# Optimization experiments

Hardware: AMD Instinct MI355X
Metric: run time of the kernel (lower is better)

## Reference

```python
import jax, jax.numpy as jnp
import numpy as np

M = 8      # quantization steps
K = 256    # codewords per step
D = 128    # vector dim
H = 256    # hidden dim of residual MLP
S = M - 1  # number of neural steps (steps 1..M-1)
L = 2      # residual blocks per step
BEAM = 16  # beam width (cfg.B)
A = 8      # substep shortlist size (n_codes)
B = 2048   # batch


def setup_inputs() -> dict:
    key = jax.random.key(0)
    ks = jax.random.split(key, 16)
    sc = 0.05
    f32 = jnp.float32
    return {
        "x": jax.random.normal(ks[0], (B, D), f32),
        "codebook": jax.random.normal(ks[1], (M, K, D), f32) * sc,
        "codebook_rq": jax.random.normal(ks[2], (S, K, D), f32) * sc,
        "W_in": jax.random.normal(ks[3], (S, D, H), f32) * (D ** -0.5),
        "b_in": jnp.zeros((S, H), f32),
        "W_cat": jax.random.normal(ks[4], (S, H + D, H), f32) * ((H + D) ** -0.5),
        "b_cat": jnp.zeros((S, H), f32),
        "W1": jax.random.normal(ks[5], (S, L, H, H), f32) * (H ** -0.5),
        "b1": jnp.zeros((S, L, H), f32),
        "W2": jax.random.normal(ks[6], (S, L, H, H), f32) * (H ** -0.5),
        "b2": jnp.zeros((S, L, H), f32),
        "W_out": jax.random.normal(ks[7], (S, H, D), f32) * (H ** -0.5),
        "b_out": jnp.zeros((S, D), f32),
    }


def _approx_dist(q, cb):
    # approx squared L2 dist, dropping the query norm: ||c||^2 - 2 q.c
    # q: (..., D), cb: (K, D) -> (..., K)
    return jnp.sum(cb * cb, axis=-1) - 2.0 * q @ cb.T


def reference(x, codebook, codebook_rq, W_in, b_in, W_cat, b_cat,
              W1, b1, W2, b2, W_out, b_out):
    # --- step 0: plain codebook lookup, keep top-BEAM candidates ---
    d0 = _approx_dist(x, codebook[0])                  # (B, K)
    _, codes0 = jax.lax.top_k(-d0, BEAM)               # (B, BEAM) smallest dists
    xhat = codebook[0][codes0]                          # (B, BEAM, D)
    codes_list = [codes0]

    for s in range(S):
        i_step = s + 1
        F_in = xhat.shape[1]
        F_out = BEAM if i_step < M - 1 else 1

        # substep pre-filter: shortlist A codes per beam element
        xt = x[:, None, :] - xhat                      # (B, F, D)
        d = _approx_dist(xt, codebook_rq[s])           # (B, F, K)
        _, top_c = jax.lax.top_k(-d, A)                # (B, F, A)
        cw = codebook[i_step][top_c]                   # gather: (B, F, A, D)
        cw_res = cw

        # residual MLP conditioned on current xhat
        h = cw @ W_in[s] + b_in[s]                     # (B, F, A, H)
        xb = jnp.broadcast_to(xhat[:, :, None, :], cw.shape)
        h = jnp.concatenate([h, xb], axis=-1) @ W_cat[s] + b_cat[s]
        for l in range(L):
            h = h + jax.nn.relu(h @ W1[s, l] + b1[s, l]) @ W2[s, l] + b2[s, l]
        cw = h @ W_out[s] + b_out[s] + cw_res          # res_codeword_coeff = 1.0

        # re-score flattened beam*shortlist candidates and prune to F_out
        cand = (cw + xhat[:, :, None, :]).reshape(B, F_in * A, D)
        d2 = jnp.sum(cand * cand, axis=-1) - 2.0 * jnp.einsum('bd,bkd->bk', x, cand)
        _, idx = jax.lax.top_k(-d2, F_out)             # (B, F_out)

        parent = idx // A                               # == repeat_interleave+gather
        codes_list = [jnp.take_along_axis(c, parent, axis=-1) for c in codes_list]
        codes_list.append(jnp.take_along_axis(top_c.reshape(B, F_in * A), idx, axis=-1))
        xhat = jnp.take_along_axis(cand, idx[:, :, None], axis=1)  # (B, F_out, D)

    codes_MB = jnp.stack([c[:, 0] for c in codes_list])  # (M, B), final beam = 1
    return codes_MB, xhat[:, 0, :]
```

## Files before the change

### kernel.cpp

```cpp
#include <hip/hip_runtime.h>
#include <float.h>

#define BB    2048
#define DD    128
#define KK    256
#define HH    256
#define MM    8
#define SS    7
#define BEAMW 16
#define AA    8
#define WM    32

typedef _Float16 f16x8 __attribute__((ext_vector_type(8)));
typedef float    f32x4 __attribute__((ext_vector_type(4)));

#define HSWZ(row, m) (((row) << 5) + ((((m) + ((((row) >> 3)) << 2))) & 31))

__device__ __forceinline__ int hoff(int m, int j) {
  return m * 256 + ((((j >> 3) ^ (m & 7)) << 3) | (j & 7));
}

__global__ __launch_bounds__(64) void step0_kernel(
    const float* __restrict__ x, const float* __restrict__ cb,
    float* __restrict__ xhat, int* __restrict__ codes)
{
  int b = blockIdx.x, l = threadIdx.x;
  __shared__ float xs[DD];
  xs[l]      = x[b * DD + l];
  xs[l + 64] = x[b * DD + 64 + l];
  __syncthreads();
  float dist[4];
#pragma unroll
  for (int q = 0; q < 4; ++q) {
    const float* row = cb + (size_t)(q * 64 + l) * DD;
    float dot = 0.f, nrm = 0.f;
#pragma unroll 8
    for (int d = 0; d < DD; d += 4) {
      float4 c = *(const float4*)(row + d);
      dot += c.x * xs[d] + c.y * xs[d + 1] + c.z * xs[d + 2] + c.w * xs[d + 3];
      nrm += c.x * c.x + c.y * c.y + c.z * c.z + c.w * c.w;
    }
    dist[q] = nrm - 2.f * dot;
  }
  for (int it = 0; it < BEAMW; ++it) {
    float bv = dist[0]; int bi = l;
#pragma unroll
    for (int q = 1; q < 4; ++q) {
      if (dist[q] < bv) { bv = dist[q]; bi = q * 64 + l; }
    }
#pragma unroll
    for (int mmk = 1; mmk < 64; mmk <<= 1) {
      float ov = __shfl_xor(bv, mmk);
      int   oi = __shfl_xor(bi, mmk);
      if (ov < bv || (ov == bv && oi < bi)) { bv = ov; bi = oi; }
    }
    const float* crow = cb + (size_t)bi * DD;
    float2 v = *(const float2*)(crow + l * 2);
    *(float2*)(xhat + (size_t)(b * BEAMW + it) * DD + l * 2) = v;
    if (l == 0) codes[(b * BEAMW + it) * MM] = bi;
    if (l == (bi & 63)) dist[bi >> 6] = FLT_MAX;
  }
}

__global__ __launch_bounds__(128) void rqprep_kernel(
    const float* __restrict__ rq, float* __restrict__ rqT, float* __restrict__ rqn)
{
  int k = blockIdx.x, d = threadIdx.x;
  float v = rq[k * DD + d];
  rqT[d * KK + k] = v;
  float p = v * v;
#pragma unroll
  for (int mmk = 1; mmk < 64; mmk <<= 1) p += __shfl_xor(p, mmk);
  __shared__ float ps[2];
  if ((d & 63) == 0) ps[d >> 6] = p;
  __syncthreads();
  if (d == 0) rqn[k] = ps[0] + ps[1];
}

__global__ __launch_bounds__(256) void codeterm_kernel(
    const float* __restrict__ cbstep, const float* __restrict__ Win,
    const float* __restrict__ bin, const float* __restrict__ Wcat,
    const float* __restrict__ bcat, float* __restrict__ ct)
{
  int k = blockIdx.x, j = threadIdx.x;
  __shared__ float crow[DD];
  __shared__ float h1[HH];
  if (j < DD) crow[j] = cbstep[k * DD + j];
  __syncthreads();
  float a = bin[j];
  for (int d = 0; d < DD; ++d) a += crow[d] * Win[d * HH + j];
  h1[j] = a;
  __syncthreads();
  float c = bcat[j];
  for (int t = 0; t < HH; ++t) c += h1[t] * Wcat[t * HH + j];
  ct[k * HH + j] = c;
}

__global__ __launch_bounds__(256) void wpack_kernel(
    const float* __restrict__ W1s, const float* __restrict__ W2s,
    const float* __restrict__ Wouts, const float* __restrict__ Wcat2s,
    _Float16* __restrict__ wAh, _Float16* __restrict__ wAl,
    _Float16* __restrict__ woh, _Float16* __restrict__ wol,
    _Float16* __restrict__ wch, _Float16* __restrict__ wcl)
{
  int t = blockIdx.x * 256 + threadIdx.x;
  const float* src; _Float16 *dh, *dl;
  int N, r;
  if (t < 32768) {
    int mi = t >> 13; r = t & 8191;
    src = (mi & 1 ? W2s : W1s) + (size_t)(mi >> 1) * HH * HH;
    dh = wAh + (size_t)mi * 65536; dl = wAl + (size_t)mi * 65536;
    N = 256;
  } else if (t < 36864) {
    r = t - 32768; src = Wouts; dh = woh; dl = wol; N = 128;
  } else {
    r = t - 36864; src = Wcat2s; dh = wch; dl = wcl; N = 256;
  }
  int l = r & 63;
  int nct = N >> 4;
  int c = (r >> 6) & (nct - 1);
  int q = r / (64 * nct);
  int k0 = q * 32 + (l >> 4) * 8;
  int col = c * 16 + (l & 15);
  size_t fo = (size_t)r * 8;
#pragma unroll
  for (int j = 0; j < 8; ++j) {
    float v = src[(size_t)(k0 + j) * N + col];
    _Float16 hi = (_Float16)v;
    dh[fo + j] = hi;
    dl[fo + j] = (_Float16)((v - (float)hi) * 2048.0f);
  }
}

__global__ __launch_bounds__(256) void prefilter_kernel(
    const float* __restrict__ x, const float* __restrict__ xhat,
    const float* __restrict__ rqT, const float* __restrict__ rqn,
    int* __restrict__ topc)
{
  __shared__ float xtT[DD * 32];
  __shared__ float distb[32 * KK];
  int tid = threadIdx.x;
  int bf0 = blockIdx.x * 32;
  for (int i = 0; i < 16; ++i) {
    int idx = tid + i * 256;
    int d = idx >> 5, r = idx & 31;
    int bf = bf0 + r;
    xtT[HSWZ(d, r)] = x[(bf >> 4) * DD + d] - xhat[(size_t)bf * DD + d];
  }
  __syncthreads();
  int jb = tid & 31, mb = tid >> 5;
  float acc[4][8];
#pragma unroll
  for (int i = 0; i < 4; ++i)
#pragma unroll
    for (int jj = 0; jj < 8; ++jj) acc[i][jj] = 0.f;
  for (int d = 0; d < DD; ++d) {
    float4 hv = *(float4*)&xtT[HSWZ(d, mb * 4)];
    float4 w0 = *(const float4*)&rqT[d * KK + jb * 8];
    float4 w1 = *(const float4*)&rqT[d * KK + jb * 8 + 4];
    float hvv[4] = {hv.x, hv.y, hv.z, hv.w};
    float wv[8]  = {w0.x, w0.y, w0.z, w0.w, w1.x, w1.y, w1.z, w1.w};
#pragma unroll
    for (int i = 0; i < 4; ++i)
#pragma unroll
      for (int jj = 0; jj < 8; ++jj) acc[i][jj] += hvv[i] * wv[jj];
  }
#pragma unroll
  for (int i = 0; i < 4; ++i) {
    int r = mb * 4 + i;
#pragma unroll
    for (int jj = 0; jj < 8; ++jj) {
      int k = jb * 8 + jj;
      distb[r * KK + k] = rqn[k] - 2.f * acc[i][jj];
    }
  }
  __syncthreads();
  int wv2 = tid >> 6, lane = tid & 63;
  for (int rr = 0; rr < 8; ++rr) {
    int r = wv2 * 8 + rr;
    float v[4];
#pragma unroll
    for (int q = 0; q < 4; ++q) v[q] = distb[r * KK + lane + q * 64];
    int bfr = bf0 + r;
    for (int it = 0; it < AA; ++it) {
      float bv = v[0]; int bi = lane;
#pragma unroll
      for (int q = 1; q < 4; ++q) {
        if (v[q] < bv) { bv = v[q]; bi = q * 64 + lane; }
      }
#pragma unroll
      for (int mmk = 1; mmk < 64; mmk <<= 1) {
        float ov = __shfl_xor(bv, mmk);
        int   oi = __shfl_xor(bi, mmk);
        if (ov < bv || (ov == bv && oi < bi)) { bv = ov; bi = oi; }
      }
      if (lane == (bi & 63)) v[bi >> 6] = FLT_MAX;
      if (lane == 0) topc[bfr * AA + it] = bi;
    }
  }
}

__global__ __launch_bounds__(512, 4) void mlp_kernel(
    const float* __restrict__ x, const float* __restrict__ xhat,
    const int* __restrict__ topc, const float* __restrict__ ct,
    const float* __restrict__ cbstep,
    const _Float16* __restrict__ wAh, const _Float16* __restrict__ wAl,
    const _Float16* __restrict__ woh, const _Float16* __restrict__ wol,
    const _Float16* __restrict__ wch, const _Float16* __restrict__ wcl,
    const float* __restrict__ b1a, const float* __restrict__ b2a,
    const float* __restrict__ bout,
    float* __restrict__ cand, float* __restrict__ d2g)
{
  __shared__ _Float16 hhi[WM * 256], hlo[WM * 256];
  __shared__ _Float16 xhh[16 * 128], xhl[16 * 128];
  __shared__ float xt[4 * 256];
  __shared__ float xs[DD];
  __shared__ float pd2[WM][8];
  __shared__ int   cl[WM];

  int tid = threadIdx.x;
  int l = tid & 63, w = tid >> 6;
  int lg = l >> 4, lr = l & 15;
  int bf0 = blockIdx.x * 4;
  int b = bf0 >> 4;
  const f32x4 z4 = {0.f, 0.f, 0.f, 0.f};

  if (tid < WM) cl[tid] = topc[bf0 * AA + tid];
  if (tid < DD) xs[tid] = x[b * DD + tid];
  for (int e = tid; e < 2048; e += 512) {
    int row = e >> 7, d = e & 127;
    float v = (row < 4) ? xhat[(size_t)(bf0 + row) * DD + d] : 0.f;
    _Float16 hi = (_Float16)v;
    xhh[e] = hi;
    xhl[e] = (_Float16)((v - (float)hi) * 2048.0f);
  }
  __syncthreads();

  {
    f32x4 ax1[2], ax2[2];
    ax1[0] = z4; ax1[1] = z4; ax2[0] = z4; ax2[1] = z4;
    for (int q = 0; q < 4; ++q) {
      int aoff = lr * 128 + q * 32 + lg * 8;
      f16x8 Ah = *(f16x8*)&xhh[aoff];
      f16x8 Al = *(f16x8*)&xhl[aoff];
#pragma unroll
      for (int c2 = 0; c2 < 2; ++c2) {
        size_t boff = ((size_t)(q * 16 + w * 2 + c2) * 64 + l) * 8;
        f16x8 Bh = *(const f16x8*)&wch[boff];
        f16x8 Bl = *(const f16x8*)&wcl[boff];
        ax1[c2] = __builtin_amdgcn_mfma_f32_16x16x32_f16(Ah, Bh, ax1[c2], 0, 0, 0);
        ax2[c2] = __builtin_amdgcn_mfma_f32_16x16x32_f16(Al, Bh, ax2[c2], 0, 0, 0);
        ax2[c2] = __builtin_amdgcn_mfma_f32_16x16x32_f16(Ah, Bl, ax2[c2], 0, 0, 0);
      }
    }
    if (l < 16) {
#pragma unroll
      for (int c2 = 0; c2 < 2; ++c2) {
        int j = (w * 2 + c2) * 16 + lr;
#pragma unroll
        for (int r = 0; r < 4; ++r)
          xt[r * 256 + j] = ax1[c2][r] + ax2[c2][r] * (1.0f / 2048.0f);
      }
    }
  }
  __syncthreads();

  for (int i = 0; i < 16; ++i) {
    int e = tid + i * 512;
    int m = e >> 8, j = e & 255;
    float v = ct[cl[m] * HH + j] + xt[(m >> 3) * 256 + j];
    _Float16 hi = (_Float16)v;
    int off = hoff(m, j);
    hhi[off] = hi;
    hlo[off] = (_Float16)((v - (float)hi) * 2048.0f);
  }
  __syncthreads();

  int j0 = (w * 2) * 16 + lr;
  int j1 = (w * 2 + 1) * 16 + lr;

  for (int lay = 0; lay < 2; ++lay) {
    const _Float16* W1h = wAh + (size_t)(lay * 2 + 0) * 65536;
    const _Float16* W1l = wAl + (size_t)(lay * 2 + 0) * 65536;
    const _Float16* W2h = wAh + (size_t)(lay * 2 + 1) * 65536;
    const _Float16* W2l = wAl + (size_t)(lay * 2 + 1) * 65536;
    const float* bb1 = b1a + lay * HH;
    const float* bb2 = b2a + lay * HH;

    f32x4 a1[2][2], a2[2][2];
#pragma unroll
    for (int rt = 0; rt < 2; ++rt)
#pragma unroll
      for (int c = 0; c < 2; ++c) { a1[rt][c] = z4; a2[rt][c] = z4; }
    for (int q = 0; q < 8; ++q) {
      f16x8 Bh[2], Bl[2];
#pragma unroll
      for (int c = 0; c < 2; ++c) {
        size_t boff = ((size_t)(q * 16 + w * 2 + c) * 64 + l) * 8;
        Bh[c] = *(const f16x8*)&W1h[boff];
        Bl[c] = *(const f16x8*)&W1l[boff];
      }
#pragma unroll
      for (int rt = 0; rt < 2; ++rt) {
        int arow = rt * 16 + lr;
        int aoff = arow * 256 + (((q * 4 + lg) ^ (arow & 7)) << 3);
        f16x8 Ah = *(f16x8*)&hhi[aoff];
        f16x8 Al = *(f16x8*)&hlo[aoff];
#pragma unroll
        for (int c = 0; c < 2; ++c) {
          a1[rt][c] = __builtin_amdgcn_mfma_f32_16x16x32_f16(Ah, Bh[c], a1[rt][c], 0, 0, 0);
          a2[rt][c] = __builtin_amdgcn_mfma_f32_16x16x32_f16(Al, Bh[c], a2[rt][c], 0, 0, 0);
          a2[rt][c] = __builtin_amdgcn_mfma_f32_16x16x32_f16(Ah, Bl[c], a2[rt][c], 0, 0, 0);
        }
      }
    }
#pragma unroll
    for (int rt = 0; rt < 2; ++rt)
#pragma unroll
      for (int c = 0; c < 2; ++c) {
        int j = (c == 0) ? j0 : j1;
        float bj = bb1[j];
#pragma unroll
        for (int r = 0; r < 4; ++r) {
          int m = rt * 16 + lg * 4 + r;
          float u = fmaxf(a1[rt][c][r] + a2[rt][c][r] * (1.0f / 2048.0f) + bj, 0.f);
          int off = hoff(m, j);
          float res = (float)hhi[off] + (float)hlo[off] * (1.0f / 2048.0f);
          a1[rt][c][r] = u;
          a2[rt][c][r] = res;
        }
      }
    __syncthreads();
#pragma unroll
    for (int rt = 0; rt < 2; ++rt)
#pragma unroll
      for (int c = 0; c < 2; ++c) {
        int j = (c == 0) ? j0 : j1;
#pragma unroll
        for (int r = 0; r < 4; ++r) {
          int m = rt * 16 + lg * 4 + r;
          float v = a1[rt][c][r];
          _Float16 hi = (_Float16)v;
          int off = hoff(m, j);
          hhi[off] = hi;
          hlo[off] = (_Float16)((v - (float)hi) * 2048.0f);
        }
      }
    __syncthreads();

#pragma unroll
    for (int rt = 0; rt < 2; ++rt)
#pragma unroll
      for (int c = 0; c < 2; ++c) {
        a1[rt][c] = a2[rt][c];
        a2[rt][c] = z4;
      }
    for (int q = 0; q < 8; ++q) {
      f16x8 Bh[2], Bl[2];
#pragma unroll
      for (int c = 0; c < 2; ++c) {
        size_t boff = ((size_t)(q * 16 + w * 2 + c) * 64 + l) * 8;
        Bh[c] = *(const f16x8*)&W2h[boff];
        Bl[c] = *(const f16x8*)&W2l[boff];
      }
#pragma unroll
      for (int rt = 0; rt < 2; ++rt) {
        int arow = rt * 16 + lr;
        int aoff = arow * 256 + (((q * 4 + lg) ^ (arow & 7)) << 3);
        f16x8 Ah = *(f16x8*)&hhi[aoff];
        f16x8 Al = *(f16x8*)&hlo[aoff];
#pragma unroll
        for (int c = 0; c < 2; ++c) {
          a1[rt][c] = __builtin_amdgcn_mfma_f32_16x16x32_f16(Ah, Bh[c], a1[rt][c], 0, 0, 0);
          a2[rt][c] = __builtin_amdgcn_mfma_f32_16x16x32_f16(Al, Bh[c], a2[rt][c], 0, 0, 0);
          a2[rt][c] = __builtin_amdgcn_mfma_f32_16x16x32_f16(Ah, Bl[c], a2[rt][c], 0, 0, 0);
        }
      }
    }
#pragma unroll
    for (int rt = 0; rt < 2; ++rt)
#pragma unroll
      for (int c = 0; c < 2; ++c) {
        int j = (c == 0) ? j0 : j1;
        float bj = bb2[j];
#pragma unroll
        for (int r = 0; r < 4; ++r)
          a1[rt][c][r] += a2[rt][c][r] * (1.0f / 2048.0f) + bj;
      }
    __syncthreads();
#pragma unroll
    for (int rt = 0; rt < 2; ++rt)
#pragma unroll
      for (int c = 0; c < 2; ++c) {
        int j = (c == 0) ? j0 : j1;
#pragma unroll
        for (int r = 0; r < 4; ++r) {
          int m = rt * 16 + lg * 4 + r;
          float v = a1[rt][c][r];
          _Float16 hi = (_Float16)v;
          int off = hoff(m, j);
          hhi[off] = hi;
          hlo[off] = (_Float16)((v - (float)hi) * 2048.0f);
        }
      }
    __syncthreads();
  }

  f32x4 o1[2], o2[2];
  o1[0] = z4; o1[1] = z4; o2[0] = z4; o2[1] = z4;
  for (int q = 0; q < 8; ++q) {
    size_t boff = ((size_t)(q * 8 + w) * 64 + l) * 8;
    f16x8 Bh = *(const f16x8*)&woh[boff];
    f16x8 Bl = *(const f16x8*)&wol[boff];
#pragma unroll
    for (int rt = 0; rt < 2; ++rt) {
      int arow = rt * 16 + lr;
      int aoff = arow * 256 + (((q * 4 + lg) ^ (arow & 7)) << 3);
      f16x8 Ah = *(f16x8*)&hhi[aoff];
      f16x8 Al = *(f16x8*)&hlo[aoff];
      o1[rt] = __builtin_amdgcn_mfma_f32_16x16x32_f16(Ah, Bh, o1[rt], 0, 0, 0);
      o2[rt] = __builtin_amdgcn_mfma_f32_16x16x32_f16(Al, Bh, o2[rt], 0, 0, 0);
      o2[rt] = __builtin_amdgcn_mfma_f32_16x16x32_f16(Ah, Bl, o2[rt], 0, 0, 0);
    }
  }
  int ci0 = (blockIdx.x & 3) * WM;
  int d = w * 16 + lr;
  float bo = bout[d];
  float xsd = xs[d];
#pragma unroll
  for (int rt = 0; rt < 2; ++rt) {
    float p[4];
#pragma unroll
    for (int r = 0; r < 4; ++r) {
      int m = rt * 16 + lg * 4 + r;
      float v = o1[rt][r] + o2[rt][r] * (1.0f / 2048.0f) + bo
              + cbstep[(size_t)cl[m] * DD + d]
              + xhat[(size_t)(bf0 + (m >> 3)) * DD + d];
      cand[((size_t)(b * 128 + ci0 + m)) * DD + d] = v;
      p[r] = v * (v - 2.f * xsd);
    }
#pragma unroll
    for (int mk = 1; mk < 16; mk <<= 1) {
#pragma unroll
      for (int r = 0; r < 4; ++r) p[r] += __shfl_xor(p[r], mk);
    }
    if (lr == 0) {
#pragma unroll
      for (int r = 0; r < 4; ++r) pd2[rt * 16 + lg * 4 + r][w] = p[r];
    }
  }
  __syncthreads();
  if (tid < WM) {
    float s = 0.f;
#pragma unroll
    for (int ww = 0; ww < 8; ++ww) s += pd2[tid][ww];
    d2g[b * 128 + ci0 + tid] = s;
  }
}

__global__ __launch_bounds__(64) void topk_update_kernel(
    const float* __restrict__ d2g, const float* __restrict__ cand,
    const int* __restrict__ codes_in, const int* __restrict__ topc,
    float* __restrict__ xhat_out, int* __restrict__ codes_out,
    int fout, int spos)
{
  int b = blockIdx.x, lane = threadIdx.x;
  float v0 = d2g[b * 128 + lane];
  float v1 = d2g[b * 128 + 64 + lane];
  for (int r = 0; r < fout; ++r) {
    float bv = v0; int bi = lane;
    if (v1 < bv) { bv = v1; bi = 64 + lane; }
#pragma unroll
    for (int mmk = 1; mmk < 64; mmk <<= 1) {
      float ov = __shfl_xor(bv, mmk);
      int   oi = __shfl_xor(bi, mmk);
      if (ov < bv || (ov == bv && oi < bi)) { bv = ov; bi = oi; }
    }
    int parent = bi >> 3, a = bi & 7;
    if (lane < MM) {
      int valc = (lane == spos) ? topc[(b * BEAMW + parent) * AA + a]
                                : codes_in[(b * BEAMW + parent) * MM + lane];
      codes_out[(b * BEAMW + r) * MM + lane] = valc;
    }
    const float* src = cand + ((size_t)(b * 128 + bi)) * DD;
    float2 t = *(const float2*)(src + lane * 2);
    *(float2*)(xhat_out + (size_t)(b * BEAMW + r) * DD + lane * 2) = t;
    if (bi < 64) { if (lane == bi) v0 = FLT_MAX; }
    else         { if (lane == bi - 64) v1 = FLT_MAX; }
  }
}

__global__ __launch_bounds__(64) void finalize_kernel(
    const int* __restrict__ codes_fin, const float* __restrict__ xhat_fin,
    float* __restrict__ out)
{
  int b = blockIdx.x, lane = threadIdx.x;
  float2 t = *(const float2*)(xhat_fin + (size_t)(b * BEAMW) * DD + lane * 2);
  *(float2*)(out + (size_t)MM * BB + (size_t)b * DD + lane * 2) = t;
  if (lane < MM) out[lane * BB + b] = (float)codes_fin[(b * BEAMW) * MM + lane];
}

extern "C" void kernel_launch(void* const* d_in, const int* in_sizes, int n_in,
                              void* d_out, int out_size, void* d_ws, size_t ws_size,
                              hipStream_t stream)
{
  (void)in_sizes; (void)n_in; (void)out_size; (void)ws_size;
  const float* x    = (const float*)d_in[0];
  const float* cb   = (const float*)d_in[1];
  const float* rq   = (const float*)d_in[2];
  const float* Win  = (const float*)d_in[3];
  const float* bin  = (const float*)d_in[4];
  const float* Wcat = (const float*)d_in[5];
  const float* bcat = (const float*)d_in[6];
  const float* W1   = (const float*)d_in[7];
  const float* b1   = (const float*)d_in[8];
  const float* W2   = (const float*)d_in[9];
  const float* b2   = (const float*)d_in[10];
  const float* Wout = (const float*)d_in[11];
  const float* bout = (const float*)d_in[12];
  float* out = (float*)d_out;

  char* ws = (char*)d_ws;
  size_t off = 0;
  auto alloc = [&](size_t bytes) -> void* {
    void* p = ws + off;
    off += (bytes + 255) & ~(size_t)255;
    return p;
  };
  float* X0    = (float*)alloc((size_t)BB * BEAMW * DD * 4);
  float* X1    = (float*)alloc((size_t)BB * BEAMW * DD * 4);
  int*   C0    = (int*)  alloc((size_t)BB * BEAMW * MM * 4);
  int*   C1    = (int*)  alloc((size_t)BB * BEAMW * MM * 4);
  int*   tc    = (int*)  alloc((size_t)BB * BEAMW * AA * 4);
  float* rqT   = (float*)alloc((size_t)DD * KK * 4);
  float* rqn   = (float*)alloc((size_t)KK * 4);
  float* ct    = (float*)alloc((size_t)KK * HH * 4);
  float* d2b   = (float*)alloc((size_t)BB * 128 * 4);
  float* candb = (float*)alloc((size_t)BB * 128 * DD * 4);
  _Float16* wAh = (_Float16*)alloc((size_t)4 * 65536 * 2);
  _Float16* wAl = (_Float16*)alloc((size_t)4 * 65536 * 2);
  _Float16* woh = (_Float16*)alloc((size_t)32768 * 2);
  _Float16* wol = (_Float16*)alloc((size_t)32768 * 2);
  _Float16* wch = (_Float16*)alloc((size_t)32768 * 2);
  _Float16* wcl = (_Float16*)alloc((size_t)32768 * 2);

  step0_kernel<<<BB, 64, 0, stream>>>(x, cb, X0, C0);
  float* Xc = X0; float* Xn = X1;
  int* Cc = C0; int* Cn = C1;
  for (int s = 0; s < SS; ++s) {
    wpack_kernel<<<160, 256, 0, stream>>>(
        W1 + (size_t)s * 2 * HH * HH, W2 + (size_t)s * 2 * HH * HH,
        Wout + (size_t)s * HH * DD,
        Wcat + (size_t)s * 384 * HH + (size_t)256 * HH,
        wAh, wAl, woh, wol, wch, wcl);
    rqprep_kernel<<<KK, DD, 0, stream>>>(rq + (size_t)s * KK * DD, rqT, rqn);
    codeterm_kernel<<<KK, HH, 0, stream>>>(cb + (size_t)(s + 1) * KK * DD,
        Win + (size_t)s * DD * HH, bin + (size_t)s * HH,
        Wcat + (size_t)s * 384 * HH, bcat + (size_t)s * HH, ct);
    prefilter_kernel<<<(BB * BEAMW) / 32, 256, 0, stream>>>(x, Xc, rqT, rqn, tc);
    mlp_kernel<<<(BB * BEAMW * AA) / WM, 512, 0, stream>>>(x, Xc, tc, ct,
        cb + (size_t)(s + 1) * KK * DD,
        wAh, wAl, woh, wol, wch, wcl,
        b1 + (size_t)s * 2 * HH, b2 + (size_t)s * 2 * HH,
        bout + (size_t)s * DD,
        candb, d2b);
    int fo = (s < SS - 1) ? BEAMW : 1;
    topk_update_kernel<<<BB, 64, 0, stream>>>(d2b, candb, Cc, tc, Xn, Cn, fo, s + 1);
    { float* t = Xc; Xc = Xn; Xn = t; }
    { int* t = Cc; Cc = Cn; Cn = t; }
  }
  finalize_kernel<<<BB, 64, 0, stream>>>(Cc, Xc, out);
}
```

Baseline: 4.870 ms.

## Hoist xhat W_cat term into separate kernel and double MLP rows per block

Moves the xhat·W_cat projection out of the MLP kernel into a new xterm kernel that computes it once per beam row with full 16-row MFMA tiles, instead of padding 4 rows to 16 inside each MLP block. The MLP kernel now processes 64 candidate rows per block instead of 32, so each weight fragment loaded from global memory feeds twice as many MFMAs. The cost is an extra launch, a global round trip for the xterm buffer, twice the LDS for the hidden state, and more accumulator registers, which may lower occupancy.

```diff
diff --git a/kernel.cpp b/kernel.cpp
--- a/kernel.cpp
+++ b/kernel.cpp
@@ -9,7 +9,7 @@
 #define SS    7
 #define BEAMW 16
 #define AA    8
-#define WM    32
+#define WM    64
 
 typedef _Float16 f16x8 __attribute__((ext_vector_type(8)));
 typedef float    f32x4 __attribute__((ext_vector_type(4)));
@@ -132,6 +132,52 @@
   }
 }
 
+__global__ __launch_bounds__(256) void xterm_kernel(
+    const float* __restrict__ xhat,
+    const _Float16* __restrict__ wch, const _Float16* __restrict__ wcl,
+    float* __restrict__ xtg)
+{
+  int tid = threadIdx.x;
+  int l = tid & 63, w = tid >> 6;
+  int lg = l >> 4, lr = l & 15;
+  int r0 = blockIdx.x * 16;
+  const f32x4 z4 = {0.f, 0.f, 0.f, 0.f};
+  f32x4 a1[4], a2[4];
+#pragma unroll
+  for (int c = 0; c < 4; ++c) { a1[c] = z4; a2[c] = z4; }
+  for (int q = 0; q < 4; ++q) {
+    const float* ap = xhat + (size_t)(r0 + lr) * DD + q * 32 + lg * 8;
+    float4 f0 = *(const float4*)ap;
+    float4 f1 = *(const float4*)(ap + 4);
+    float fv[8] = {f0.x, f0.y, f0.z, f0.w, f1.x, f1.y, f1.z, f1.w};
+    f16x8 Ah, Al;
+#pragma unroll
+    for (int j = 0; j < 8; ++j) {
+      _Float16 hi = (_Float16)fv[j];
+      Ah[j] = hi;
+      Al[j] = (_Float16)((fv[j] - (float)hi) * 2048.0f);
+    }
+#pragma unroll
+    for (int c = 0; c < 4; ++c) {
+      size_t boff = ((size_t)(q * 16 + w * 4 + c) * 64 + l) * 8;
+      f16x8 Bh = *(const f16x8*)&wch[boff];
+      f16x8 Bl = *(const f16x8*)&wcl[boff];
+      a1[c] = __builtin_amdgcn_mfma_f32_16x16x32_f16(Ah, Bh, a1[c], 0, 0, 0);
+      a2[c] = __builtin_amdgcn_mfma_f32_16x16x32_f16(Al, Bh, a2[c], 0, 0, 0);
+      a2[c] = __builtin_amdgcn_mfma_f32_16x16x32_f16(Ah, Bl, a2[c], 0, 0, 0);
+    }
+  }
+#pragma unroll
+  for (int c = 0; c < 4; ++c) {
+    int col = (w * 4 + c) * 16 + lr;
+#pragma unroll
+    for (int r = 0; r < 4; ++r) {
+      int row = r0 + lg * 4 + r;
+      xtg[(size_t)row * 256 + col] = a1[c][r] + a2[c][r] * (1.0f / 2048.0f);
+    }
+  }
+}
+
 __global__ __launch_bounds__(256) void prefilter_kernel(
     const float* __restrict__ x, const float* __restrict__ xhat,
     const float* __restrict__ rqT, const float* __restrict__ rqn,
@@ -203,17 +249,14 @@
 __global__ __launch_bounds__(512, 4) void mlp_kernel(
     const float* __restrict__ x, const float* __restrict__ xhat,
     const int* __restrict__ topc, const float* __restrict__ ct,
-    const float* __restrict__ cbstep,
+    const float* __restrict__ cbstep, const float* __restrict__ xtg,
     const _Float16* __restrict__ wAh, const _Float16* __restrict__ wAl,
     const _Float16* __restrict__ woh, const _Float16* __restrict__ wol,
-    const _Float16* __restrict__ wch, const _Float16* __restrict__ wcl,
     const float* __restrict__ b1a, const float* __restrict__ b2a,
     const float* __restrict__ bout,
     float* __restrict__ cand, float* __restrict__ d2g)
 {
   __shared__ _Float16 hhi[WM * 256], hlo[WM * 256];
-  __shared__ _Float16 xhh[16 * 128], xhl[16 * 128];
-  __shared__ float xt[4 * 256];
   __shared__ float xs[DD];
   __shared__ float pd2[WM][8];
   __shared__ int   cl[WM];
@@ -221,54 +264,18 @@
   int tid = threadIdx.x;
   int l = tid & 63, w = tid >> 6;
   int lg = l >> 4, lr = l & 15;
-  int bf0 = blockIdx.x * 4;
+  int bf0 = blockIdx.x * 8;
   int b = bf0 >> 4;
   const f32x4 z4 = {0.f, 0.f, 0.f, 0.f};
 
   if (tid < WM) cl[tid] = topc[bf0 * AA + tid];
   if (tid < DD) xs[tid] = x[b * DD + tid];
-  for (int e = tid; e < 2048; e += 512) {
-    int row = e >> 7, d = e & 127;
-    float v = (row < 4) ? xhat[(size_t)(bf0 + row) * DD + d] : 0.f;
-    _Float16 hi = (_Float16)v;
-    xhh[e] = hi;
-    xhl[e] = (_Float16)((v - (float)hi) * 2048.0f);
-  }
-  __syncthreads();
-
-  {
-    f32x4 ax1[2], ax2[2];
-    ax1[0] = z4; ax1[1] = z4; ax2[0] = z4; ax2[1] = z4;
-    for (int q = 0; q < 4; ++q) {
-      int aoff = lr * 128 + q * 32 + lg * 8;
-      f16x8 Ah = *(f16x8*)&xhh[aoff];
-      f16x8 Al = *(f16x8*)&xhl[aoff];
-#pragma unroll
-      for (int c2 = 0; c2 < 2; ++c2) {
-        size_t boff = ((size_t)(q * 16 + w * 2 + c2) * 64 + l) * 8;
-        f16x8 Bh = *(const f16x8*)&wch[boff];
-        f16x8 Bl = *(const f16x8*)&wcl[boff];
-        ax1[c2] = __builtin_amdgcn_mfma_f32_16x16x32_f16(Ah, Bh, ax1[c2], 0, 0, 0);
-        ax2[c2] = __builtin_amdgcn_mfma_f32_16x16x32_f16(Al, Bh, ax2[c2], 0, 0, 0);
-        ax2[c2] = __builtin_amdgcn_mfma_f32_16x16x32_f16(Ah, Bl, ax2[c2], 0, 0, 0);
-      }
-    }
-    if (l < 16) {
-#pragma unroll
-      for (int c2 = 0; c2 < 2; ++c2) {
-        int j = (w * 2 + c2) * 16 + lr;
-#pragma unroll
-        for (int r = 0; r < 4; ++r)
-          xt[r * 256 + j] = ax1[c2][r] + ax2[c2][r] * (1.0f / 2048.0f);
-      }
-    }
-  }
-  __syncthreads();
-
-  for (int i = 0; i < 16; ++i) {
+  __syncthreads();
+
+  for (int i = 0; i < 32; ++i) {
     int e = tid + i * 512;
     int m = e >> 8, j = e & 255;
-    float v = ct[cl[m] * HH + j] + xt[(m >> 3) * 256 + j];
+    float v = ct[cl[m] * HH + j] + xtg[(size_t)(bf0 + (m >> 3)) * 256 + j];
     _Float16 hi = (_Float16)v;
     int off = hoff(m, j);
     hhi[off] = hi;
@@ -287,9 +294,9 @@
     const float* bb1 = b1a + lay * HH;
     const float* bb2 = b2a + lay * HH;
 
-    f32x4 a1[2][2], a2[2][2];
-#pragma unroll
-    for (int rt = 0; rt < 2; ++rt)
+    f32x4 a1[4][2], a2[4][2];
+#pragma unroll
+    for (int rt = 0; rt < 4; ++rt)
 #pragma unroll
       for (int c = 0; c < 2; ++c) { a1[rt][c] = z4; a2[rt][c] = z4; }
     for (int q = 0; q < 8; ++q) {
@@ -301,7 +308,7 @@
         Bl[c] = *(const f16x8*)&W1l[boff];
       }
 #pragma unroll
-      for (int rt = 0; rt < 2; ++rt) {
+      for (int rt = 0; rt < 4; ++rt) {
         int arow = rt * 16 + lr;
         int aoff = arow * 256 + (((q * 4 + lg) ^ (arow & 7)) << 3);
         f16x8 Ah = *(f16x8*)&hhi[aoff];
@@ -315,7 +322,7 @@
       }
     }
 #pragma unroll
-    for (int rt = 0; rt < 2; ++rt)
+    for (int rt = 0; rt < 4; ++rt)
 #pragma unroll
       for (int c = 0; c < 2; ++c) {
         int j = (c == 0) ? j0 : j1;
@@ -332,7 +339,7 @@
       }
     __syncthreads();
 #pragma unroll
-    for (int rt = 0; rt < 2; ++rt)
+    for (int rt = 0; rt < 4; ++rt)
 #pragma unroll
       for (int c = 0; c < 2; ++c) {
         int j = (c == 0) ? j0 : j1;
@@ -349,7 +356,7 @@
     __syncthreads();
 
 #pragma unroll
-    for (int rt = 0; rt < 2; ++rt)
+    for (int rt = 0; rt < 4; ++rt)
 #pragma unroll
       for (int c = 0; c < 2; ++c) {
         a1[rt][c] = a2[rt][c];
@@ -364,7 +371,7 @@
         Bl[c] = *(const f16x8*)&W2l[boff];
       }
 #pragma unroll
-      for (int rt = 0; rt < 2; ++rt) {
+      for (int rt = 0; rt < 4; ++rt) {
         int arow = rt * 16 + lr;
         int aoff = arow * 256 + (((q * 4 + lg) ^ (arow & 7)) << 3);
         f16x8 Ah = *(f16x8*)&hhi[aoff];
@@ -378,7 +385,7 @@
       }
     }
 #pragma unroll
-    for (int rt = 0; rt < 2; ++rt)
+    for (int rt = 0; rt < 4; ++rt)
 #pragma unroll
       for (int c = 0; c < 2; ++c) {
         int j = (c == 0) ? j0 : j1;
@@ -389,7 +396,7 @@
       }
     __syncthreads();
 #pragma unroll
-    for (int rt = 0; rt < 2; ++rt)
+    for (int rt = 0; rt < 4; ++rt)
 #pragma unroll
       for (int c = 0; c < 2; ++c) {
         int j = (c == 0) ? j0 : j1;
@@ -406,14 +413,15 @@
     __syncthreads();
   }
 
-  f32x4 o1[2], o2[2];
-  o1[0] = z4; o1[1] = z4; o2[0] = z4; o2[1] = z4;
+  f32x4 o1[4], o2[4];
+#pragma unroll
+  for (int rt = 0; rt < 4; ++rt) { o1[rt] = z4; o2[rt] = z4; }
   for (int q = 0; q < 8; ++q) {
     size_t boff = ((size_t)(q * 8 + w) * 64 + l) * 8;
     f16x8 Bh = *(const f16x8*)&woh[boff];
     f16x8 Bl = *(const f16x8*)&wol[boff];
 #pragma unroll
-    for (int rt = 0; rt < 2; ++rt) {
+    for (int rt = 0; rt < 4; ++rt) {
       int arow = rt * 16 + lr;
       int aoff = arow * 256 + (((q * 4 + lg) ^ (arow & 7)) << 3);
       f16x8 Ah = *(f16x8*)&hhi[aoff];
@@ -423,12 +431,12 @@
       o2[rt] = __builtin_amdgcn_mfma_f32_16x16x32_f16(Ah, Bl, o2[rt], 0, 0, 0);
     }
   }
-  int ci0 = (blockIdx.x & 3) * WM;
+  int ci0 = (blockIdx.x & 1) * WM;
   int d = w * 16 + lr;
   float bo = bout[d];
   float xsd = xs[d];
 #pragma unroll
-  for (int rt = 0; rt < 2; ++rt) {
+  for (int rt = 0; rt < 4; ++rt) {
     float p[4];
 #pragma unroll
     for (int r = 0; r < 4; ++r) {
@@ -537,6 +545,7 @@
   float* ct    = (float*)alloc((size_t)KK * HH * 4);
   float* d2b   = (float*)alloc((size_t)BB * 128 * 4);
   float* candb = (float*)alloc((size_t)BB * 128 * DD * 4);
+  float* xtg   = (float*)alloc((size_t)BB * BEAMW * 256 * 4);
   _Float16* wAh = (_Float16*)alloc((size_t)4 * 65536 * 2);
   _Float16* wAl = (_Float16*)alloc((size_t)4 * 65536 * 2);
   _Float16* woh = (_Float16*)alloc((size_t)32768 * 2);
@@ -558,9 +567,10 @@
         Win + (size_t)s * DD * HH, bin + (size_t)s * HH,
         Wcat + (size_t)s * 384 * HH, bcat + (size_t)s * HH, ct);
     prefilter_kernel<<<(BB * BEAMW) / 32, 256, 0, stream>>>(x, Xc, rqT, rqn, tc);
+    xterm_kernel<<<(BB * BEAMW) / 16, 256, 0, stream>>>(Xc, wch, wcl, xtg);
     mlp_kernel<<<(BB * BEAMW * AA) / WM, 512, 0, stream>>>(x, Xc, tc, ct,
-        cb + (size_t)(s + 1) * KK * DD,
-        wAh, wAl, woh, wol, wch, wcl,
+        cb + (size_t)(s + 1) * KK * DD, xtg,
+        wAh, wAl, woh, wol,
         b1 + (size_t)s * 2 * HH, b2 + (size_t)s * 2 * HH,
         bout + (size_t)s * DD,
         candb, d2b);
```

Measured after the change: 7.694 ms. 58.0% more time.
